# Optimization experiments

Measured on AMD Instinct MI355X. Metric: run time of the kernel, lower is better.

## Reference

```python
import jax, jax.numpy as jnp
import numpy as np

B, N, DIM, H = 4, 2048, 64, 8
SCALE = DIM ** -0.5  # qk_scale defaults to head_dim**-0.5 with head_dim = dim


def setup_inputs() -> dict:
    key = jax.random.key(0)
    k1, k2, k3 = jax.random.split(key, 3)
    x = jax.random.normal(k1, (B, N, DIM), dtype=jnp.float32)
    Wqkv = jax.random.normal(k2, (DIM, 3 * H * DIM), dtype=jnp.float32) * (DIM ** -0.5)
    Wproj = jax.random.normal(k3, (H * DIM, DIM), dtype=jnp.float32) * ((H * DIM) ** -0.5)
    bproj = jnp.zeros((DIM,), dtype=jnp.float32)
    return {"x": x, "Wqkv": Wqkv, "Wproj": Wproj, "bproj": bproj}


def reference(x, Wqkv, Wproj, bproj):
    Bx, Nx, C = x.shape
    # qkv: [B,N,3*H*C] -> [B,N,3,H,C] -> (3,B,H,N,C)
    qkv = (x @ Wqkv).reshape(Bx, Nx, 3, H, C).transpose(2, 0, 3, 1, 4)
    q, k, v = qkv[0], qkv[1], qkv[2]
    # scores: [B,H,N,N]
    attn = jax.nn.softmax(jnp.einsum('bhnc,bhmc->bhnm', q, k) * SCALE, axis=-1)
    out = jnp.einsum('bhnm,bhmc->bhnc', attn, v)  # [B,H,N,C]
    out = out.transpose(0, 2, 1, 3).reshape(Bx, Nx, H * C)  # [B,N,H*C]
    return out @ Wproj + bproj  # [B,N,C]
```

## Files before the change

kernel.cpp:

```cpp
#include <hip/hip_runtime.h>

#define NB 4
#define SEQ 2048
#define CD 64
#define NHEAD 8
#define BHN (NB * NHEAD)
#define ROWS (NB * SEQ)
#define HC 512

#define QSCALE 0.18033688011112042f
#define SHIFT  23.083120654223414f

typedef float f32x4 __attribute__((ext_vector_type(4)));
typedef short s16x8 __attribute__((ext_vector_type(8)));
typedef unsigned short u16;
typedef unsigned int u32;

__device__ __forceinline__ u16 f2bf(float x) {
  union { float f; unsigned u; } v; v.f = x;
  unsigned r = v.u + 0x7FFFu + ((v.u >> 16) & 1u);
  return (u16)(r >> 16);
}

__device__ __forceinline__ float fast_exp2(float x) {
#if __has_builtin(__builtin_amdgcn_exp2f)
  return __builtin_amdgcn_exp2f(x);
#else
  return exp2f(x);
#endif
}

__device__ __forceinline__ u32 bitsf(float x) {
  union { float f; u32 u; } v; v.f = x; return v.u;
}

__device__ __forceinline__ u32 pack_trunc(float a, float b) {
#if __has_builtin(__builtin_amdgcn_perm)
  return __builtin_amdgcn_perm(bitsf(b), bitsf(a), 0x07060302u);
#else
  return (bitsf(a) >> 16) | (bitsf(b) & 0xFFFF0000u);
#endif
}

__device__ __forceinline__ f32x4 mfma_bf16(s16x8 a, s16x8 b, f32x4 c) {
  return __builtin_amdgcn_mfma_f32_16x16x32_bf16(a, b, c, 0, 0, 0);
}

typedef __attribute__((address_space(1))) const u32* gp1;
typedef __attribute__((address_space(3))) u32* lp3;
__device__ __forceinline__ void dma16(const void* g, void* l) {
  __builtin_amdgcn_global_load_lds((gp1)g, (lp3)l, 16, 0, 0);
}

__global__ void __launch_bounds__(256) prep_kernel(
    const float* __restrict__ Wqkv, const float* __restrict__ Wproj,
    u16* __restrict__ WT, u16* __restrict__ WpT) {
  const int idx = blockIdx.x * 256 + threadIdx.x;
  if (idx < 64 * 1536) {
    const int k = idx / 1536, n = idx % 1536;
    WT[n * CD + k] = f2bf(Wqkv[idx]);
  }
  if (idx < 512 * 64) {
    const int k = idx >> 6, c = idx & 63;
    WpT[c * HC + k] = f2bf(Wproj[idx]);
  }
}

__global__ void __launch_bounds__(256) qkv_kernel(
    const float* __restrict__ x, const u16* __restrict__ WT,
    u16* __restrict__ Q, u16* __restrict__ K, u16* __restrict__ Vt) {
  __shared__ __align__(16) u16 xs[64 * 72];
  __shared__ __align__(16) u16 wts[192 * 72];

  const int t = threadIdx.x;
  const int w = t >> 6, lane = t & 63, quad = lane >> 4, c16 = lane & 15;
  const int rb = blockIdx.x * 64;
  const int c0 = blockIdx.y * 192;

  {
    const int row = t >> 2, cc0 = (t & 3) * 16;
    const float* xp = x + (size_t)(rb + row) * CD + cc0;
    union { u16 u[16]; int4 v[2]; } bx;
#pragma unroll
    for (int j = 0; j < 16; j += 4) {
      float4 xv = *(const float4*)(xp + j);
      bx.u[j] = f2bf(xv.x); bx.u[j + 1] = f2bf(xv.y);
      bx.u[j + 2] = f2bf(xv.z); bx.u[j + 3] = f2bf(xv.w);
    }
    *(int4*)&xs[row * 72 + cc0] = bx.v[0];
    *(int4*)&xs[row * 72 + cc0 + 8] = bx.v[1];
  }
#pragma unroll
  for (int pass = 0; pass < 3; ++pass) {
    const int row = pass * 64 + (t >> 2), cc0 = (t & 3) * 16;
    const u16* src = WT + (size_t)(c0 + row) * CD + cc0;
    *(int4*)&wts[row * 72 + cc0] = *(const int4*)src;
    *(int4*)&wts[row * 72 + cc0 + 8] = *(const int4*)(src + 8);
  }
  __syncthreads();

  s16x8 af[2];
#pragma unroll
  for (int kc = 0; kc < 2; ++kc)
    af[kc] = *(const s16x8*)&xs[(w * 16 + c16) * 72 + kc * 32 + quad * 8];

  f32x4 acc[12];
#pragma unroll
  for (int nb = 0; nb < 12; ++nb) acc[nb] = (f32x4){0.f, 0.f, 0.f, 0.f};

#pragma unroll
  for (int nb = 0; nb < 12; ++nb) {
#pragma unroll
    for (int kc = 0; kc < 2; ++kc) {
      const s16x8 bf_ =
          *(const s16x8*)&wts[(nb * 16 + c16) * 72 + kc * 32 + quad * 8];
      acc[nb] = mfma_bf16(af[kc], bf_, acc[nb]);
    }
  }

  const int rw = rb + w * 16;
  const int b = rw >> 11;
  const int nn0 = rw & (SEQ - 1);
#pragma unroll
  for (int nb = 0; nb < 12; ++nb) {
    const int cb = c0 + nb * 16;
    const int three = cb >> 9;
    const int h = (cb >> 6) & 7;
    const int ccb = cb & 63;
    const int bhv = b * NHEAD + h;
    if (three == 2) {
      union { u16 u[4]; uint2 v; } pk;
#pragma unroll
      for (int i = 0; i < 4; ++i) pk.u[i] = f2bf(acc[nb][i]);
      const size_t off = (size_t)bhv * (SEQ * CD) + (size_t)(nn0 >> 5) * 2048 +
                         (size_t)(ccb + c16) * 32 + (rw & 31) + quad * 4;
      *(uint2*)(Vt + off) = pk.v;
    } else {
      u16* dstp = (three == 0) ? Q : K;
      const float scl = (three == 0) ? QSCALE : 1.0f;
#pragma unroll
      for (int i = 0; i < 4; ++i) {
        const int nn = nn0 + quad * 4 + i;
        dstp[((size_t)bhv * SEQ + nn) * CD + ccb + c16] = f2bf(acc[nb][i] * scl);
      }
    }
  }
}

__global__ void __launch_bounds__(128, 2) attn_kernel(
    const u16* __restrict__ Q, const u16* __restrict__ K,
    const u16* __restrict__ Vt, u16* __restrict__ O) {
  __shared__ __align__(16) u16 smem[17664];

  const int t = threadIdx.x;
  const int w = t >> 6, lane = t & 63, quad = lane >> 4, c16 = lane & 15;
  const int bh = blockIdx.y;
  const int q0 = blockIdx.x * 64;
  const int kt0 = w * (SEQ / 2);

  u16* KsW = smem + w * 8192;
  u16* VsW = smem + w * 8192 + 4096;
  u16* Pw  = smem + 16384 + w * 640;

  const u16* Qb = Q + (size_t)bh * SEQ * CD;
  const u16* Kb = K + (size_t)bh * SEQ * CD;
  const u16* Vb = Vt + (size_t)bh * SEQ * CD;

  s16x8 qfb[4][2];
#pragma unroll
  for (int qb = 0; qb < 4; ++qb)
#pragma unroll
    for (int cc = 0; cc < 2; ++cc)
      qfb[qb][cc] = *(const s16x8*)(Qb + (size_t)(q0 + qb * 16 + c16) * CD +
                                    cc * 32 + quad * 8);

  s16x8 onesf;
  {
    const short one = (c16 == 0) ? (short)0x3F80 : (short)0;
#pragma unroll
    for (int j = 0; j < 8; ++j) onesf[j] = one;
  }

  f32x4 o[4][4], osum[4];
#pragma unroll
  for (int qb = 0; qb < 4; ++qb) {
    osum[qb] = (f32x4){0.f, 0.f, 0.f, 0.f};
#pragma unroll
    for (int cb = 0; cb < 4; ++cb) o[qb][cb] = (f32x4){0.f, 0.f, 0.f, 0.f};
  }

  const int krl = lane >> 3, kcl = (lane & 7) ^ ((lane >> 3) & 7);
  const int vrl = lane >> 2, vcl = (lane & 3) ^ ((lane >> 3) & 3);

  int kOff[2][2], vOff[4];
#pragma unroll
  for (int kb = 0; kb < 2; ++kb)
#pragma unroll
    for (int cc = 0; cc < 2; ++cc)
      kOff[kb][cc] = (kb * 16 + c16) * 64 + (((cc * 4 + quad) ^ (c16 & 7)) * 8);
#pragma unroll
  for (int cb = 0; cb < 4; ++cb)
    vOff[cb] = (cb * 16 + c16) * 32 + ((quad ^ ((c16 >> 1) & 3)) * 8);

#define STAGE_TILE(buf_, kt_)                                                  \
  {                                                                            \
    const u16* ksrc = Kb + (size_t)(kt_) * CD;                                 \
    _Pragma("unroll") for (int d = 0; d < 4; ++d)                              \
        dma16(ksrc + (size_t)(d * 8 + krl) * CD + kcl * 8,                     \
              KsW + (buf_) * 2048 + d * 512);                                  \
    const u16* vsrc = Vb + (size_t)((kt_) >> 5) * 2048;                        \
    _Pragma("unroll") for (int d = 0; d < 4; ++d)                              \
        dma16(vsrc + (size_t)(d * 16 + vrl) * 32 + vcl * 8,                    \
              VsW + (buf_) * 2048 + d * 512);                                  \
  }

  STAGE_TILE(0, kt0)

  for (int it = 0; it < 32; ++it) {
    const int bs = it & 1;
    __syncthreads();

    if (it + 1 < 32) STAGE_TILE(bs ^ 1, kt0 + (it + 1) * 32)

    s16x8 kf[2][2], vf[4];
#pragma unroll
    for (int kb = 0; kb < 2; ++kb)
#pragma unroll
      for (int cc = 0; cc < 2; ++cc)
        kf[kb][cc] = *(const s16x8*)&KsW[bs * 2048 + kOff[kb][cc]];
#pragma unroll
    for (int cb = 0; cb < 4; ++cb)
      vf[cb] = *(const s16x8*)&VsW[bs * 2048 + vOff[cb]];

#pragma unroll
    for (int qb = 0; qb < 4; ++qb) {
#pragma unroll
      for (int kb = 0; kb < 2; ++kb) {
        f32x4 s = (f32x4){-SHIFT, -SHIFT, -SHIFT, -SHIFT};
        s = mfma_bf16(kf[kb][0], qfb[qb][0], s);
        s = mfma_bf16(kf[kb][1], qfb[qb][1], s);
        uint2 pk;
        pk.x = pack_trunc(fast_exp2(s[0]), fast_exp2(s[1]));
        pk.y = pack_trunc(fast_exp2(s[2]), fast_exp2(s[3]));
        *(uint2*)&Pw[c16 * 40 + kb * 16 + quad * 4] = pk;
      }
      const s16x8 pf = *(const s16x8*)&Pw[c16 * 40 + quad * 8];
#pragma unroll
      for (int cb = 0; cb < 4; ++cb)
        o[qb][cb] = mfma_bf16(pf, vf[cb], o[qb][cb]);
      osum[qb] = mfma_bf16(pf, onesf, osum[qb]);
    }
  }
#undef STAGE_TILE

  float* X  = (float*)(smem + 8192);
  float* Lx = (float*)(smem + 16384 + 640);

  if (w == 1) {
#pragma unroll
    for (int qb = 0; qb < 4; ++qb) {
#pragma unroll
      for (int cb = 0; cb < 4; ++cb)
#pragma unroll
        for (int i = 0; i < 4; ++i)
          X[(qb * 16 + quad * 4 + i) * 64 + cb * 16 + c16] = o[qb][cb][i];
      if (c16 == 0)
#pragma unroll
        for (int i = 0; i < 4; ++i)
          Lx[qb * 16 + quad * 4 + i] = osum[qb][i];
    }
  }
  __syncthreads();
  if (w == 0) {
    const int b = bh >> 3, h = bh & 7;
#pragma unroll
    for (int qb = 0; qb < 4; ++qb) {
#pragma unroll
      for (int i = 0; i < 4; ++i) {
        const float l0 = __shfl(osum[qb][i], lane & 48);
        const int qq = qb * 16 + quad * 4 + i;
        const float inv = 1.0f / (l0 + Lx[qq]);
        const int q = q0 + qq;
        u16* dst = O + ((size_t)(b * SEQ + q)) * HC + h * CD;
#pragma unroll
        for (int cb = 0; cb < 4; ++cb)
          dst[cb * 16 + c16] =
              f2bf((o[qb][cb][i] + X[qq * 64 + cb * 16 + c16]) * inv);
      }
    }
  }
}

__global__ void __launch_bounds__(256) proj_kernel(
    const u16* __restrict__ O, const u16* __restrict__ WpT,
    const float* __restrict__ bias, float* __restrict__ out) {
  __shared__ __align__(16) u16 Ls[16 * 520];
  __shared__ __align__(16) float Cred[4][64][20];
  const int t = threadIdx.x;
  const int w = t >> 6, lane = t & 63, quad = lane >> 4, c16 = lane & 15;
  const int r0 = blockIdx.x * 16;

  s16x8 wf[4][4];
#pragma unroll
  for (int kc = 0; kc < 4; ++kc)
#pragma unroll
    for (int nb = 0; nb < 4; ++nb)
      wf[kc][nb] = *(const s16x8*)(WpT + (size_t)(nb * 16 + c16) * HC +
                                   w * 128 + kc * 32 + quad * 8);

  {
    const int row = t >> 4, cg = (t & 15) * 8;
#pragma unroll
    for (int p = 0; p < 4; ++p)
      *(int4*)&Ls[row * 520 + p * 128 + cg] =
          *(const int4*)(O + (size_t)(r0 + row) * HC + p * 128 + cg);
  }
  __syncthreads();

  f32x4 acc[4];
#pragma unroll
  for (int nb = 0; nb < 4; ++nb) acc[nb] = (f32x4){0.f, 0.f, 0.f, 0.f};
#pragma unroll
  for (int kc = 0; kc < 4; ++kc) {
    const s16x8 af =
        *(const s16x8*)&Ls[c16 * 520 + w * 128 + kc * 32 + quad * 8];
#pragma unroll
    for (int nb = 0; nb < 4; ++nb)
      acc[nb] = mfma_bf16(af, wf[kc][nb], acc[nb]);
  }

#pragma unroll
  for (int nb = 0; nb < 4; ++nb)
    *(f32x4*)&Cred[w][nb * 16 + c16][quad * 4] = acc[nb];
  __syncthreads();

  const int col = t & 63, rbase = (t >> 6) * 4;
  const float bv = bias[col];
#pragma unroll
  for (int j = 0; j < 4; ++j) {
    const int r = rbase + j;
    out[(size_t)(r0 + r) * CD + col] = Cred[0][col][r] + Cred[1][col][r] +
                                       Cred[2][col][r] + Cred[3][col][r] + bv;
  }
}

extern "C" void kernel_launch(void* const* d_in, const int* in_sizes, int n_in,
                              void* d_out, int out_size, void* d_ws, size_t ws_size,
                              hipStream_t stream) {
  (void)in_sizes; (void)n_in; (void)out_size; (void)ws_size;
  const float* x     = (const float*)d_in[0];
  const float* Wqkv  = (const float*)d_in[1];
  const float* Wproj = (const float*)d_in[2];
  const float* bproj = (const float*)d_in[3];
  float* out = (float*)d_out;

  u16* WT  = (u16*)d_ws;
  u16* WpT = WT + 1536 * CD;
  u16* Qw  = WpT + CD * HC;
  u16* Kw  = Qw + (size_t)BHN * SEQ * CD;
  u16* Vtw = Kw + (size_t)BHN * SEQ * CD;
  u16* Ow  = Vtw + (size_t)BHN * SEQ * CD;

  prep_kernel<<<384, 256, 0, stream>>>(Wqkv, Wproj, WT, WpT);
  qkv_kernel<<<dim3(128, 8), 256, 0, stream>>>(x, WT, Qw, Kw, Vtw);
  attn_kernel<<<dim3(32, 32), 128, 0, stream>>>(Qw, Kw, Vtw, Ow);
  proj_kernel<<<512, 256, 0, stream>>>(Ow, WpT, bproj, out);
}
```

Baseline: 126.1 us.

## Replace per-tile barrier with wave-local waitcnt and vectorize QKV/proj weight stores

In the attention loop, each wave stages its own K/V tiles into a private LDS region. The block-wide __syncthreads per tile is therefore replaced with an s_waitcnt on outstanding vector-memory loads, and the last tile is peeled out of the loop. The QKV kernel now issues the MFMA per output block and swaps operands for Q/K, so each lane writes four packed bf16 values with a single 8-byte store instead of four scalar stores. The projection weights are pre-arranged in MFMA fragment order so each lane loads a fragment with one contiguous read. The risk is that removing the barrier leaves correctness dependent on the hand-encoded waitcnt values and on the per-wave buffer ownership.

```diff
diff --git a/kernel.cpp b/kernel.cpp
--- a/kernel.cpp
+++ b/kernel.cpp
@@ -42,6 +42,10 @@
 #endif
 }
 
+__device__ __forceinline__ u32 pack_rne(float a, float b) {
+  return (u32)f2bf(a) | ((u32)f2bf(b) << 16);
+}
+
 __device__ __forceinline__ f32x4 mfma_bf16(s16x8 a, s16x8 b, f32x4 c) {
   return __builtin_amdgcn_mfma_f32_16x16x32_bf16(a, b, c, 0, 0, 0);
 }
@@ -54,15 +58,20 @@
 
 __global__ void __launch_bounds__(256) prep_kernel(
     const float* __restrict__ Wqkv, const float* __restrict__ Wproj,
-    u16* __restrict__ WT, u16* __restrict__ WpT) {
+    u16* __restrict__ WT, u16* __restrict__ WpF) {
   const int idx = blockIdx.x * 256 + threadIdx.x;
   if (idx < 64 * 1536) {
     const int k = idx / 1536, n = idx % 1536;
     WT[n * CD + k] = f2bf(Wqkv[idx]);
   }
-  if (idx < 512 * 64) {
-    const int k = idx >> 6, c = idx & 63;
-    WpT[c * HC + k] = f2bf(Wproj[idx]);
+  if (idx < 64 * 512) {
+    const int f = idx >> 9;
+    const int lane = (idx >> 3) & 63;
+    const int j = idx & 7;
+    const int kcg = f >> 2, nb = f & 3;
+    const int col = nb * 16 + (lane & 15);
+    const int k = kcg * 32 + (lane >> 4) * 8 + j;
+    WpF[idx] = f2bf(Wproj[k * 64 + col]);
   }
 }
 
@@ -104,23 +113,10 @@
   for (int kc = 0; kc < 2; ++kc)
     af[kc] = *(const s16x8*)&xs[(w * 16 + c16) * 72 + kc * 32 + quad * 8];
 
-  f32x4 acc[12];
-#pragma unroll
-  for (int nb = 0; nb < 12; ++nb) acc[nb] = (f32x4){0.f, 0.f, 0.f, 0.f};
-
-#pragma unroll
-  for (int nb = 0; nb < 12; ++nb) {
-#pragma unroll
-    for (int kc = 0; kc < 2; ++kc) {
-      const s16x8 bf_ =
-          *(const s16x8*)&wts[(nb * 16 + c16) * 72 + kc * 32 + quad * 8];
-      acc[nb] = mfma_bf16(af[kc], bf_, acc[nb]);
-    }
-  }
-
   const int rw = rb + w * 16;
   const int b = rw >> 11;
   const int nn0 = rw & (SEQ - 1);
+
 #pragma unroll
   for (int nb = 0; nb < 12; ++nb) {
     const int cb = c0 + nb * 16;
@@ -128,21 +124,32 @@
     const int h = (cb >> 6) & 7;
     const int ccb = cb & 63;
     const int bhv = b * NHEAD + h;
+    s16x8 bf_[2];
+#pragma unroll
+    for (int kc = 0; kc < 2; ++kc)
+      bf_[kc] = *(const s16x8*)&wts[(nb * 16 + c16) * 72 + kc * 32 + quad * 8];
+
     if (three == 2) {
-      union { u16 u[4]; uint2 v; } pk;
-#pragma unroll
-      for (int i = 0; i < 4; ++i) pk.u[i] = f2bf(acc[nb][i]);
+      f32x4 acc = (f32x4){0.f, 0.f, 0.f, 0.f};
+#pragma unroll
+      for (int kc = 0; kc < 2; ++kc) acc = mfma_bf16(af[kc], bf_[kc], acc);
+      uint2 pk;
+      pk.x = pack_rne(acc[0], acc[1]);
+      pk.y = pack_rne(acc[2], acc[3]);
       const size_t off = (size_t)bhv * (SEQ * CD) + (size_t)(nn0 >> 5) * 2048 +
                          (size_t)(ccb + c16) * 32 + (rw & 31) + quad * 4;
-      *(uint2*)(Vt + off) = pk.v;
+      *(uint2*)(Vt + off) = pk;
     } else {
+      f32x4 acc = (f32x4){0.f, 0.f, 0.f, 0.f};
+#pragma unroll
+      for (int kc = 0; kc < 2; ++kc) acc = mfma_bf16(bf_[kc], af[kc], acc);
       u16* dstp = (three == 0) ? Q : K;
       const float scl = (three == 0) ? QSCALE : 1.0f;
-#pragma unroll
-      for (int i = 0; i < 4; ++i) {
-        const int nn = nn0 + quad * 4 + i;
-        dstp[((size_t)bhv * SEQ + nn) * CD + ccb + c16] = f2bf(acc[nb][i] * scl);
-      }
+      uint2 pk;
+      pk.x = pack_rne(acc[0] * scl, acc[1] * scl);
+      pk.y = pack_rne(acc[2] * scl, acc[3] * scl);
+      *(uint2*)(dstp + ((size_t)bhv * SEQ + nn0 + c16) * CD + ccb + quad * 4) =
+          pk;
     }
   }
 }
@@ -214,44 +221,43 @@
               VsW + (buf_) * 2048 + d * 512);                                  \
   }
 
+#define COMPUTE_TILE(bs_)                                                      \
+  {                                                                            \
+    s16x8 kf[2][2], vf[4];                                                     \
+    _Pragma("unroll") for (int kb = 0; kb < 2; ++kb)                           \
+        _Pragma("unroll") for (int cc = 0; cc < 2; ++cc)                       \
+            kf[kb][cc] = *(const s16x8*)&KsW[(bs_) * 2048 + kOff[kb][cc]];     \
+    _Pragma("unroll") for (int cb = 0; cb < 4; ++cb)                           \
+        vf[cb] = *(const s16x8*)&VsW[(bs_) * 2048 + vOff[cb]];                 \
+    _Pragma("unroll") for (int qb = 0; qb < 4; ++qb) {                         \
+      _Pragma("unroll") for (int kb = 0; kb < 2; ++kb) {                       \
+        f32x4 s = (f32x4){-SHIFT, -SHIFT, -SHIFT, -SHIFT};                     \
+        s = mfma_bf16(kf[kb][0], qfb[qb][0], s);                               \
+        s = mfma_bf16(kf[kb][1], qfb[qb][1], s);                               \
+        uint2 pk;                                                              \
+        pk.x = pack_trunc(fast_exp2(s[0]), fast_exp2(s[1]));                   \
+        pk.y = pack_trunc(fast_exp2(s[2]), fast_exp2(s[3]));                   \
+        *(uint2*)&Pw[c16 * 40 + kb * 16 + quad * 4] = pk;                      \
+      }                                                                        \
+      const s16x8 pf = *(const s16x8*)&Pw[c16 * 40 + quad * 8];                \
+      _Pragma("unroll") for (int cb = 0; cb < 4; ++cb)                         \
+          o[qb][cb] = mfma_bf16(pf, vf[cb], o[qb][cb]);                        \
+      osum[qb] = mfma_bf16(pf, onesf, osum[qb]);                               \
+    }                                                                          \
+  }
+
   STAGE_TILE(0, kt0)
 
-  for (int it = 0; it < 32; ++it) {
+  for (int it = 0; it < 31; ++it) {
     const int bs = it & 1;
-    __syncthreads();
-
-    if (it + 1 < 32) STAGE_TILE(bs ^ 1, kt0 + (it + 1) * 32)
-
-    s16x8 kf[2][2], vf[4];
-#pragma unroll
-    for (int kb = 0; kb < 2; ++kb)
-#pragma unroll
-      for (int cc = 0; cc < 2; ++cc)
-        kf[kb][cc] = *(const s16x8*)&KsW[bs * 2048 + kOff[kb][cc]];
-#pragma unroll
-    for (int cb = 0; cb < 4; ++cb)
-      vf[cb] = *(const s16x8*)&VsW[bs * 2048 + vOff[cb]];
-
-#pragma unroll
-    for (int qb = 0; qb < 4; ++qb) {
-#pragma unroll
-      for (int kb = 0; kb < 2; ++kb) {
-        f32x4 s = (f32x4){-SHIFT, -SHIFT, -SHIFT, -SHIFT};
-        s = mfma_bf16(kf[kb][0], qfb[qb][0], s);
-        s = mfma_bf16(kf[kb][1], qfb[qb][1], s);
-        uint2 pk;
-        pk.x = pack_trunc(fast_exp2(s[0]), fast_exp2(s[1]));
-        pk.y = pack_trunc(fast_exp2(s[2]), fast_exp2(s[3]));
-        *(uint2*)&Pw[c16 * 40 + kb * 16 + quad * 4] = pk;
-      }
-      const s16x8 pf = *(const s16x8*)&Pw[c16 * 40 + quad * 8];
-#pragma unroll
-      for (int cb = 0; cb < 4; ++cb)
-        o[qb][cb] = mfma_bf16(pf, vf[cb], o[qb][cb]);
-      osum[qb] = mfma_bf16(pf, onesf, osum[qb]);
-    }
-  }
+    STAGE_TILE(bs ^ 1, kt0 + (it + 1) * 32)
+    __builtin_amdgcn_s_waitcnt(0x0F78);
+    COMPUTE_TILE(bs)
+  }
+  __builtin_amdgcn_s_waitcnt(0x0F70);
+  COMPUTE_TILE(1)
 #undef STAGE_TILE
+#undef COMPUTE_TILE
 
   float* X  = (float*)(smem + 8192);
   float* Lx = (float*)(smem + 16384 + 640);
@@ -292,7 +298,7 @@
 }
 
 __global__ void __launch_bounds__(256) proj_kernel(
-    const u16* __restrict__ O, const u16* __restrict__ WpT,
+    const u16* __restrict__ O, const u16* __restrict__ WpF,
     const float* __restrict__ bias, float* __restrict__ out) {
   __shared__ __align__(16) u16 Ls[16 * 520];
   __shared__ __align__(16) float Cred[4][64][20];
@@ -305,8 +311,8 @@
   for (int kc = 0; kc < 4; ++kc)
 #pragma unroll
     for (int nb = 0; nb < 4; ++nb)
-      wf[kc][nb] = *(const s16x8*)(WpT + (size_t)(nb * 16 + c16) * HC +
-                                   w * 128 + kc * 32 + quad * 8);
+      wf[kc][nb] = *(const s16x8*)(WpF + ((((w * 4 + kc) * 4 + nb) << 9) +
+                                          lane * 8));
 
   {
     const int row = t >> 4, cg = (t & 15) * 8;
@@ -355,14 +361,14 @@
   float* out = (float*)d_out;
 
   u16* WT  = (u16*)d_ws;
-  u16* WpT = WT + 1536 * CD;
-  u16* Qw  = WpT + CD * HC;
+  u16* WpF = WT + 1536 * CD;
+  u16* Qw  = WpF + CD * HC;
   u16* Kw  = Qw + (size_t)BHN * SEQ * CD;
   u16* Vtw = Kw + (size_t)BHN * SEQ * CD;
   u16* Ow  = Vtw + (size_t)BHN * SEQ * CD;
 
-  prep_kernel<<<384, 256, 0, stream>>>(Wqkv, Wproj, WT, WpT);
+  prep_kernel<<<384, 256, 0, stream>>>(Wqkv, Wproj, WT, WpF);
   qkv_kernel<<<dim3(128, 8), 256, 0, stream>>>(x, WT, Qw, Kw, Vtw);
   attn_kernel<<<dim3(32, 32), 128, 0, stream>>>(Qw, Kw, Vtw, Ow);
-  proj_kernel<<<512, 256, 0, stream>>>(Ow, WpT, bproj, out);
-}
+  proj_kernel<<<512, 256, 0, stream>>>(Ow, WpF, bproj, out);
+}
```

Measured after the change: 123.1 us. 1.02x faster.
